# Performance work log

Measured on AMD Instinct MI355X. Metric: run time of the kernel, lower is better.

## Reference

```python
import jax, jax.numpy as jnp
import numpy as np

B, N, H, W, NHOR = 4096, 128, 128, 64, 3

def setup_inputs() -> dict:
    key = jax.random.key(0)
    ks = jax.random.split(key, 11)
    s = 1.0 / np.sqrt(H)
    return {
        "embeddings": jax.random.normal(ks[0], (B, H), jnp.float32),
        "sensor_embeddings": jax.random.normal(ks[1], (B, N, H), jnp.float32),
        "sensor_logits": jax.random.normal(ks[2], (B, N), jnp.float32),
        "fc1_w": jax.random.normal(ks[3], (H, H), jnp.float32) * s,
        "fc1_b": jax.random.normal(ks[4], (H,), jnp.float32) * s,
        "fc2_w": jax.random.normal(ks[5], (NHOR * N, H), jnp.float32) * s,
        "fc2_b": jax.random.normal(ks[6], (NHOR * N,), jnp.float32) * s,
        "rw1": jax.random.normal(ks[7], (N, H, H), jnp.float32) * s,
        "rb1": jax.random.normal(ks[8], (N, H), jnp.float32) * s,
        "rw2": jax.random.normal(ks[9], (N, H, W), jnp.float32) * s,
        "rb2": jax.random.normal(ks[10], (N, W), jnp.float32) * s,
    }

def reference(embeddings, sensor_embeddings, sensor_logits,
              fc1_w, fc1_b, fc2_w, fc2_b, rw1, rb1, rw2, rb2):
    # Forecasting head: Linear -> ReLU -> (Dropout: identity in eval) -> Linear
    h = jax.nn.relu(embeddings @ fc1_w.T + fc1_b)              # (B, H)
    forecast = (h @ fc2_w.T + fc2_b).reshape(-1, NHOR, N)      # (B, NHOR, N)
    # Reconstruction heads: per-node MLPs batched as stacked GEMMs
    hn = jax.nn.relu(jnp.einsum('bnh,nhk->bnk', sensor_embeddings, rw1) + rb1)  # (B, N, H)
    recon = jnp.einsum('bnk,nkw->bnw', hn, rw2) + rb2          # (B, N, W)
    reconstruction = jnp.transpose(recon, (0, 2, 1))           # (B, W, N), matches torch.stack(dim=2)
    return (sensor_logits, forecast, reconstruction)
```

## Files before the change

### kernel.cpp

```cpp
#include <hip/hip_runtime.h>
#include <hip/hip_bf16.h>
#include <stdint.h>

typedef __attribute__((ext_vector_type(8))) short bf16x8;
typedef __attribute__((ext_vector_type(4))) float f32x4;

#define DEVI static __device__ __forceinline__

static constexpr int B_SZ = 4096, N_SZ = 128, H_SZ = 128, W_SZ = 64;

static constexpr size_t OFF_W1 = 0;
static constexpr size_t OFF_W2 = OFF_W1 + 4194304;
static constexpr size_t OFF_F1 = OFF_W2 + 2097152;
static constexpr size_t OFF_F2 = OFF_F1 + 32768;
static constexpr size_t OFF_H  = OFF_F2 + 98304;

DEVI unsigned short f2bf(float f) {
  union { __hip_bfloat16 b; unsigned short u; } cv;
  cv.b = __float2bfloat16(f);
  return cv.u;
}
DEVI float bf2f(unsigned short u) {
  union { unsigned int i; float f; } cv;
  cv.i = ((unsigned int)u) << 16;
  return cv.f;
}

DEVI bf16x8 frag_ld(const unsigned char* base, int row, int kslot) {
  return *reinterpret_cast<const bf16x8*>(base + row * 256 + (((kslot ^ (row & 7)) << 4)));
}
DEVI bf16x8 gfrag_ld(const unsigned char* base, int row, int kslot) {
  return *reinterpret_cast<const bf16x8*>(base + row * 256 + (kslot << 4));
}

DEVI void stage_f32_tile(const float* src, int row_stride, unsigned char* dst, int tid, int nrows) {
  for (int t = tid; t < nrows * 16; t += 256) {
    int row = t >> 4, s = t & 15;
    const float* p = src + (size_t)row * row_stride + s * 8;
    union { unsigned short u[8]; uint4 v; } pk;
#pragma unroll
    for (int j = 0; j < 8; ++j) pk.u[j] = f2bf(p[j]);
    *reinterpret_cast<uint4*>(dst + row * 256 + ((s ^ (row & 7)) << 4)) = pk.v;
  }
}

__global__ __launch_bounds__(256) void prep_kernel(const float* __restrict__ rw1,
                                                   const float* __restrict__ rw2,
                                                   const float* __restrict__ fc1w,
                                                   const float* __restrict__ fc2w,
                                                   unsigned char* __restrict__ ws) {
  const int T_W1 = 128 * 128 * 16;
  const int T_W2 = 128 * 64 * 16;
  const int T_F1 = 128 * 16;
  const int T_F2 = 384 * 16;
  int id = blockIdx.x * 256 + threadIdx.x;
  if (id < T_W1) {
    int c = id & 127, rest = id >> 7;
    int s = rest & 15, n = rest >> 4;
    const float* src = rw1 + (size_t)n * 16384 + (size_t)(s * 8) * 128 + c;
    union { unsigned short u[8]; uint4 v; } pk;
#pragma unroll
    for (int j = 0; j < 8; ++j) pk.u[j] = f2bf(src[(size_t)j * 128]);
    size_t dst = OFF_W1 + ((size_t)n * 128 + c) * 256 + (size_t)(s << 4);
    *reinterpret_cast<uint4*>(ws + dst) = pk.v;
    return;
  }
  id -= T_W1;
  if (id < T_W2) {
    int w = id & 63, rest = id >> 6;
    int s = rest & 15, n = rest >> 4;
    const float* src = rw2 + (size_t)n * 8192 + (size_t)(s * 8) * 64 + w;
    union { unsigned short u[8]; uint4 v; } pk;
#pragma unroll
    for (int j = 0; j < 8; ++j) pk.u[j] = f2bf(src[(size_t)j * 64]);
    size_t dst = OFF_W2 + ((size_t)n * 64 + w) * 256 + (size_t)(s << 4);
    *reinterpret_cast<uint4*>(ws + dst) = pk.v;
    return;
  }
  id -= T_W2;
  if (id < T_F1) {
    int s = id & 15, o = id >> 4;
    const float* src = fc1w + (size_t)o * 128 + s * 8;
    union { unsigned short u[8]; uint4 v; } pk;
#pragma unroll
    for (int j = 0; j < 8; ++j) pk.u[j] = f2bf(src[j]);
    *reinterpret_cast<uint4*>(ws + OFF_F1 + (size_t)o * 256 + ((s ^ (o & 7)) << 4)) = pk.v;
    return;
  }
  id -= T_F1;
  if (id < T_F2) {
    int s = id & 15, o = id >> 4;
    const float* src = fc2w + (size_t)o * 128 + s * 8;
    union { unsigned short u[8]; uint4 v; } pk;
#pragma unroll
    for (int j = 0; j < 8; ++j) pk.u[j] = f2bf(src[j]);
    *reinterpret_cast<uint4*>(ws + OFF_F2 + (size_t)o * 256 + ((s ^ (o & 7)) << 4)) = pk.v;
  }
}

__global__ __launch_bounds__(256, 2) void recon_kernel(const float* __restrict__ se,
                                                       const float* __restrict__ rb1,
                                                       const float* __restrict__ rb2,
                                                       const unsigned char* __restrict__ ws,
                                                       float* __restrict__ out3) {
  __shared__ unsigned char sSE[2][16384];
  __shared__ unsigned char sHN[16384];

  const int tid = threadIdx.x;
  const int n = blockIdx.x;
  const int btg = blockIdx.y;
  const int b0 = btg * 512;

  const int wave = tid >> 6, lane = tid & 63;
  const int wm = wave >> 1, wq = wave & 1;
  const int lr = lane & 15, lk = lane >> 4;

  const unsigned char* w1b = ws + OFF_W1 + (size_t)n * 32768;
  const unsigned char* w2b = ws + OFF_W2 + (size_t)n * 16384;
  bf16x8 w1f[4][4], w2f[2][4];
#pragma unroll
  for (int m = 0; m < 4; ++m)
#pragma unroll
    for (int kk = 0; kk < 4; ++kk)
      w1f[m][kk] = gfrag_ld(w1b, wm * 64 + m * 16 + lr, kk * 4 + lk);
#pragma unroll
  for (int m = 0; m < 2; ++m)
#pragma unroll
    for (int kk = 0; kk < 4; ++kk)
      w2f[m][kk] = gfrag_ld(w2b, wm * 32 + m * 16 + lr, kk * 4 + lk);

  float bias1[4][4], bias2[2][4];
#pragma unroll
  for (int m = 0; m < 4; ++m)
#pragma unroll
    for (int j = 0; j < 4; ++j) bias1[m][j] = rb1[(size_t)n * 128 + wm * 64 + m * 16 + lk * 4 + j];
#pragma unroll
  for (int m = 0; m < 2; ++m)
#pragma unroll
    for (int j = 0; j < 4; ++j) bias2[m][j] = rb2[(size_t)n * 64 + wm * 32 + m * 16 + lk * 4 + j];

  stage_f32_tile(se + ((size_t)b0 * 128 + n) * 128, 128 * 128, sSE[0], tid, 64);
  unsigned short* outus = reinterpret_cast<unsigned short*>(out3);
  __syncthreads();

  float4 fra[4], frb[4];

  for (int t = 0; t < 8; ++t) {
    unsigned char* bufc = sSE[t & 1];
    unsigned char* bufn = sSE[(t + 1) & 1];

    if (t < 7) {
      const float* sb = se + ((size_t)(b0 + (t + 1) * 64) * 128 + n) * 128;
#pragma unroll
      for (int k = 0; k < 4; ++k) {
        int c = tid + k * 256;
        int row = c >> 4, s = c & 15;
        const float* p = sb + (size_t)row * 16384 + s * 8;
        fra[k] = *reinterpret_cast<const float4*>(p);
        frb[k] = *reinterpret_cast<const float4*>(p + 4);
      }
    }

    f32x4 acc[4][2] = {};
#pragma unroll
    for (int kk = 0; kk < 4; ++kk) {
      const int slot = kk * 4 + lk;
      bf16x8 bv[2];
#pragma unroll
      for (int q = 0; q < 2; ++q) bv[q] = frag_ld(bufc, wq * 32 + q * 16 + lr, slot);
#pragma unroll
      for (int m = 0; m < 4; ++m)
#pragma unroll
        for (int q = 0; q < 2; ++q)
          acc[m][q] = __builtin_amdgcn_mfma_f32_16x16x32_bf16(w1f[m][kk], bv[q], acc[m][q], 0, 0, 0);
    }

#pragma unroll
    for (int m = 0; m < 4; ++m) {
      const int k0 = wm * 64 + m * 16 + lk * 4;
      const int s16 = k0 >> 3, half = (k0 >> 2) & 1;
#pragma unroll
      for (int q = 0; q < 2; ++q) {
        const int b = wq * 32 + q * 16 + lr;
        union { unsigned short u[4]; uint2 v; } pk;
#pragma unroll
        for (int j = 0; j < 4; ++j) {
          float v = acc[m][q][j] + bias1[m][j];
          v = v > 0.f ? v : 0.f;
          pk.u[j] = f2bf(v);
        }
        *reinterpret_cast<uint2*>(sHN + b * 256 + ((s16 ^ (b & 7)) << 4) + half * 8) = pk.v;
      }
    }
    __syncthreads();

    f32x4 acc2[2][2] = {};
#pragma unroll
    for (int kk = 0; kk < 4; ++kk) {
      const int slot = kk * 4 + lk;
      bf16x8 bv[2];
#pragma unroll
      for (int q = 0; q < 2; ++q) bv[q] = frag_ld(sHN, wq * 32 + q * 16 + lr, slot);
#pragma unroll
      for (int m = 0; m < 2; ++m)
#pragma unroll
        for (int q = 0; q < 2; ++q)
          acc2[m][q] = __builtin_amdgcn_mfma_f32_16x16x32_bf16(w2f[m][kk], bv[q], acc2[m][q], 0, 0, 0);
    }

    if (t < 7) {
#pragma unroll
      for (int k = 0; k < 4; ++k) {
        int c = tid + k * 256;
        int row = c >> 4, s = c & 15;
        union { unsigned short u[8]; uint4 v; } pk;
#pragma unroll
        for (int j = 0; j < 4; ++j) pk.u[j] = f2bf(fra[k][j]);
#pragma unroll
        for (int j = 0; j < 4; ++j) pk.u[4 + j] = f2bf(frb[k][j]);
        *reinterpret_cast<uint4*>(bufn + row * 256 + ((s ^ (row & 7)) << 4)) = pk.v;
      }
    }

    const int bt0 = b0 + t * 64;
#pragma unroll
    for (int m = 0; m < 2; ++m) {
      const int w0 = wm * 32 + m * 16 + lk * 4;
#pragma unroll
      for (int q = 0; q < 2; ++q) {
        const int b = bt0 + wq * 32 + q * 16 + lr;
        union { unsigned short u[4]; uint2 v; } pk;
#pragma unroll
        for (int j = 0; j < 4; ++j) pk.u[j] = f2bf(acc2[m][q][j] + bias2[m][j]);
        *reinterpret_cast<uint2*>(outus + (size_t)b * 16384 + 8192 + n * 64 + w0) = pk.v;
      }
    }
    __syncthreads();
  }
}

__global__ __launch_bounds__(256) void transpose_kernel(float* __restrict__ out3) {
  const int b = blockIdx.x, wave = threadIdx.x >> 6, lane = threadIdx.x & 63;
  const unsigned short* t = reinterpret_cast<const unsigned short*>(out3) + (size_t)b * 16384 + 8192;
  float* dst = out3 + (size_t)b * 8192;
  uint4 r[2][2];
#pragma unroll
  for (int half = 0; half < 2; ++half) {
    const int g = half * 4 + wave;
    r[half][0] = *reinterpret_cast<const uint4*>(t + lane * 64 + g * 8);
    r[half][1] = *reinterpret_cast<const uint4*>(t + (size_t)(lane + 64) * 64 + g * 8);
  }
  __syncthreads();
#pragma unroll
  for (int half = 0; half < 2; ++half) {
    const int g = half * 4 + wave;
    union { uint4 v; unsigned short u[8]; } p0, p1;
    p0.v = r[half][0];
    p1.v = r[half][1];
#pragma unroll
    for (int j = 0; j < 8; ++j) {
      dst[(g * 8 + j) * 128 + lane] = bf2f(p0.u[j]);
      dst[(g * 8 + j) * 128 + lane + 64] = bf2f(p1.u[j]);
    }
  }
}

__global__ __launch_bounds__(256) void f1_kernel(const float* __restrict__ emb,
                                                 const float* __restrict__ fc1b,
                                                 const unsigned char* __restrict__ ws,
                                                 unsigned char* __restrict__ hsw) {
  __shared__ unsigned char sA[32768];
  __shared__ unsigned char sB[32768];
  const int tid = threadIdx.x;
  const int bt = blockIdx.x;
  const int b0 = bt * 128;
  {
    const uint4* wp = reinterpret_cast<const uint4*>(ws + OFF_F1);
    uint4* d = reinterpret_cast<uint4*>(sB);
    for (int c = tid; c < 2048; c += 256) d[c] = wp[c];
  }
  stage_f32_tile(emb + (size_t)b0 * 128, 128, sA, tid, 128);
  __syncthreads();

  const int wave = tid >> 6, lane = tid & 63;
  const int wm = wave >> 1, wn = wave & 1;
  const int lr = lane & 15, lk = lane >> 4;

  f32x4 acc[4][4] = {};
#pragma unroll
  for (int kk = 0; kk < 4; ++kk) {
    bf16x8 af[4], bfv[4];
#pragma unroll
    for (int m = 0; m < 4; ++m) af[m] = frag_ld(sA, wm * 64 + m * 16 + lr, kk * 4 + lk);
#pragma unroll
    for (int q = 0; q < 4; ++q) bfv[q] = frag_ld(sB, wn * 64 + q * 16 + lr, kk * 4 + lk);
#pragma unroll
    for (int m = 0; m < 4; ++m)
#pragma unroll
      for (int q = 0; q < 4; ++q)
        acc[m][q] = __builtin_amdgcn_mfma_f32_16x16x32_bf16(af[m], bfv[q], acc[m][q], 0, 0, 0);
  }

  unsigned char* tile = hsw + (size_t)bt * 32768;
#pragma unroll
  for (int q = 0; q < 4; ++q) {
    int c = wn * 64 + q * 16 + lr;
    float bias = fc1b[c];
#pragma unroll
    for (int m = 0; m < 4; ++m) {
#pragma unroll
      for (int j = 0; j < 4; ++j) {
        int r = wm * 64 + m * 16 + lk * 4 + j;
        float v = acc[m][q][j] + bias;
        v = v > 0.f ? v : 0.f;
        *reinterpret_cast<unsigned short*>(tile + r * 256 + ((c * 2) ^ ((r & 7) << 4))) = f2bf(v);
      }
    }
  }
}

__global__ __launch_bounds__(256) void f2_kernel(const unsigned char* __restrict__ hsw,
                                                 const unsigned char* __restrict__ f2s,
                                                 const float* __restrict__ fc2b,
                                                 float* __restrict__ out2) {
  __shared__ unsigned char sA[32768];
  __shared__ unsigned char sB[32768];
  const int tid = threadIdx.x;
  const int bt = blockIdx.x;
  const int ch = blockIdx.y;
  const int b0 = bt * 128;
  {
    const uint4* ap = reinterpret_cast<const uint4*>(hsw + (size_t)bt * 32768);
    uint4* da = reinterpret_cast<uint4*>(sA);
    for (int c = tid; c < 2048; c += 256) da[c] = ap[c];
    const uint4* bp = reinterpret_cast<const uint4*>(f2s + (size_t)ch * 32768);
    uint4* db = reinterpret_cast<uint4*>(sB);
    for (int c = tid; c < 2048; c += 256) db[c] = bp[c];
  }
  __syncthreads();

  const int wave = tid >> 6, lane = tid & 63;
  const int wm = wave >> 1, wn = wave & 1;
  const int lr = lane & 15, lk = lane >> 4;

  f32x4 acc[4][4] = {};
#pragma unroll
  for (int kk = 0; kk < 4; ++kk) {
    bf16x8 af[4], bfv[4];
#pragma unroll
    for (int m = 0; m < 4; ++m) af[m] = frag_ld(sA, wm * 64 + m * 16 + lr, kk * 4 + lk);
#pragma unroll
    for (int q = 0; q < 4; ++q) bfv[q] = frag_ld(sB, wn * 64 + q * 16 + lr, kk * 4 + lk);
#pragma unroll
    for (int m = 0; m < 4; ++m)
#pragma unroll
      for (int q = 0; q < 4; ++q)
        acc[m][q] = __builtin_amdgcn_mfma_f32_16x16x32_bf16(af[m], bfv[q], acc[m][q], 0, 0, 0);
  }

#pragma unroll
  for (int q = 0; q < 4; ++q) {
    int o = ch * 128 + wn * 64 + q * 16 + lr;
    float bias = fc2b[o];
#pragma unroll
    for (int m = 0; m < 4; ++m) {
#pragma unroll
      for (int j = 0; j < 4; ++j) {
        int r = wm * 64 + m * 16 + lk * 4 + j;
        out2[(size_t)(b0 + r) * 384 + o] = acc[m][q][j] + bias;
      }
    }
  }
}

extern "C" void kernel_launch(void* const* d_in, const int* in_sizes, int n_in,
                              void* d_out, int out_size, void* d_ws, size_t ws_size,
                              hipStream_t stream) {
  const float* emb  = (const float*)d_in[0];
  const float* se   = (const float*)d_in[1];
  const float* slog = (const float*)d_in[2];
  const float* fc1w = (const float*)d_in[3];
  const float* fc1b = (const float*)d_in[4];
  const float* fc2w = (const float*)d_in[5];
  const float* fc2b = (const float*)d_in[6];
  const float* rw1  = (const float*)d_in[7];
  const float* rb1  = (const float*)d_in[8];
  const float* rw2  = (const float*)d_in[9];
  const float* rb2  = (const float*)d_in[10];
  float* out = (float*)d_out;
  unsigned char* ws = (unsigned char*)d_ws;

  hipMemcpyAsync(out, slog, (size_t)B_SZ * N_SZ * sizeof(float),
                 hipMemcpyDeviceToDevice, stream);

  prep_kernel<<<1568, 256, 0, stream>>>(rw1, rw2, fc1w, fc2w, ws);

  f1_kernel<<<32, 256, 0, stream>>>(emb, fc1b, ws, ws + OFF_H);
  f2_kernel<<<dim3(32, 3), 256, 0, stream>>>(ws + OFF_H, ws + OFF_F2, fc2b,
                                             out + (size_t)B_SZ * N_SZ);

  float* out3 = out + (size_t)B_SZ * N_SZ + (size_t)B_SZ * 384;
  recon_kernel<<<dim3(128, 8), 256, 0, stream>>>(se, rb1, rb2, ws, out3);
  transpose_kernel<<<4096, 256, 0, stream>>>(out3);
}
```

Measured before the change: 140.9 us.

## Fuse reconstruction transpose into recon kernel via per-block node-chunk tiling

The recon kernel now handles 4 consecutive nodes for a 64-row batch tile, not one node across 512 batch rows. Results are staged in a new 32KB shared buffer laid out as (batch, w, node). It then writes the transposed fp32 output directly as float4 stores, which removes the separate transpose kernel and its bf16 intermediate round-trip through global memory. In exchange, weights are reloaded per node with less reuse across batch rows, the SE buffer is single-buffered with extra barriers, and shared memory use grows, which may lower occupancy.

```diff
diff --git a/kernel.cpp b/kernel.cpp
--- a/kernel.cpp
+++ b/kernel.cpp
@@ -103,63 +103,79 @@
                                                        const float* __restrict__ rb2,
                                                        const unsigned char* __restrict__ ws,
                                                        float* __restrict__ out3) {
-  __shared__ unsigned char sSE[2][16384];
+  __shared__ unsigned char sSE[16384];
   __shared__ unsigned char sHN[16384];
+  __shared__ unsigned char sOUT[32768];
 
   const int tid = threadIdx.x;
-  const int n = blockIdx.x;
-  const int btg = blockIdx.y;
-  const int b0 = btg * 512;
+  const int id = blockIdx.x;
+  const int chunk = ((id & 7) << 2) | ((id >> 3) & 3);
+  const int btile = id >> 5;
+  const int n0 = chunk * 4;
+  const int b0 = btile * 64;
 
   const int wave = tid >> 6, lane = tid & 63;
   const int wm = wave >> 1, wq = wave & 1;
   const int lr = lane & 15, lk = lane >> 4;
 
-  const unsigned char* w1b = ws + OFF_W1 + (size_t)n * 32768;
-  const unsigned char* w2b = ws + OFF_W2 + (size_t)n * 16384;
-  bf16x8 w1f[4][4], w2f[2][4];
-#pragma unroll
-  for (int m = 0; m < 4; ++m)
-#pragma unroll
-    for (int kk = 0; kk < 4; ++kk)
-      w1f[m][kk] = gfrag_ld(w1b, wm * 64 + m * 16 + lr, kk * 4 + lk);
-#pragma unroll
-  for (int m = 0; m < 2; ++m)
-#pragma unroll
-    for (int kk = 0; kk < 4; ++kk)
-      w2f[m][kk] = gfrag_ld(w2b, wm * 32 + m * 16 + lr, kk * 4 + lk);
-
-  float bias1[4][4], bias2[2][4];
-#pragma unroll
-  for (int m = 0; m < 4; ++m)
-#pragma unroll
-    for (int j = 0; j < 4; ++j) bias1[m][j] = rb1[(size_t)n * 128 + wm * 64 + m * 16 + lk * 4 + j];
-#pragma unroll
-  for (int m = 0; m < 2; ++m)
-#pragma unroll
-    for (int j = 0; j < 4; ++j) bias2[m][j] = rb2[(size_t)n * 64 + wm * 32 + m * 16 + lk * 4 + j];
-
-  stage_f32_tile(se + ((size_t)b0 * 128 + n) * 128, 128 * 128, sSE[0], tid, 64);
-  unsigned short* outus = reinterpret_cast<unsigned short*>(out3);
+  stage_f32_tile(se + ((size_t)b0 * 128 + n0) * 128, 128 * 128, sSE, tid, 64);
   __syncthreads();
 
   float4 fra[4], frb[4];
 
-  for (int t = 0; t < 8; ++t) {
-    unsigned char* bufc = sSE[t & 1];
-    unsigned char* bufn = sSE[(t + 1) & 1];
-
-    if (t < 7) {
-      const float* sb = se + ((size_t)(b0 + (t + 1) * 64) * 128 + n) * 128;
-#pragma unroll
-      for (int k = 0; k < 4; ++k) {
-        int c = tid + k * 256;
-        int row = c >> 4, s = c & 15;
-        const float* p = sb + (size_t)row * 16384 + s * 8;
-        fra[k] = *reinterpret_cast<const float4*>(p);
-        frb[k] = *reinterpret_cast<const float4*>(p + 4);
-      }
-    }
+  auto issue_pref = [&](int n) {
+    const float* sb = se + ((size_t)b0 * 128 + n) * 128;
+#pragma unroll
+    for (int k = 0; k < 4; ++k) {
+      int c = tid + k * 256;
+      int row = c >> 4, s = c & 15;
+      const float* p = sb + (size_t)row * 16384 + s * 8;
+      fra[k] = *reinterpret_cast<const float4*>(p);
+      frb[k] = *reinterpret_cast<const float4*>(p + 4);
+    }
+  };
+  auto write_pref = [&]() {
+#pragma unroll
+    for (int k = 0; k < 4; ++k) {
+      int c = tid + k * 256;
+      int row = c >> 4, s = c & 15;
+      union { unsigned short u[8]; uint4 v; } pk;
+#pragma unroll
+      for (int j = 0; j < 4; ++j) pk.u[j] = f2bf(fra[k][j]);
+#pragma unroll
+      for (int j = 0; j < 4; ++j) pk.u[4 + j] = f2bf(frb[k][j]);
+      *reinterpret_cast<uint4*>(sSE + row * 256 + ((s ^ (row & 7)) << 4)) = pk.v;
+    }
+  };
+
+#pragma unroll 1
+  for (int nl = 0; nl < 4; ++nl) {
+    const int n = n0 + nl;
+
+    const unsigned char* w1b = ws + OFF_W1 + (size_t)n * 32768;
+    const unsigned char* w2b = ws + OFF_W2 + (size_t)n * 16384;
+    bf16x8 w1f[4][4], w2f[2][4];
+#pragma unroll
+    for (int m = 0; m < 4; ++m)
+#pragma unroll
+      for (int kk = 0; kk < 4; ++kk)
+        w1f[m][kk] = gfrag_ld(w1b, wm * 64 + m * 16 + lr, kk * 4 + lk);
+#pragma unroll
+    for (int m = 0; m < 2; ++m)
+#pragma unroll
+      for (int kk = 0; kk < 4; ++kk)
+        w2f[m][kk] = gfrag_ld(w2b, wm * 32 + m * 16 + lr, kk * 4 + lk);
+    float bias1[4][4], bias2[2][4];
+#pragma unroll
+    for (int m = 0; m < 4; ++m)
+#pragma unroll
+      for (int j = 0; j < 4; ++j) bias1[m][j] = rb1[(size_t)n * 128 + wm * 64 + m * 16 + lk * 4 + j];
+#pragma unroll
+    for (int m = 0; m < 2; ++m)
+#pragma unroll
+      for (int j = 0; j < 4; ++j) bias2[m][j] = rb2[(size_t)n * 64 + wm * 32 + m * 16 + lk * 4 + j];
+
+    if (nl == 0) issue_pref(n0 + 1);
 
     f32x4 acc[4][2] = {};
 #pragma unroll
@@ -167,13 +183,14 @@
       const int slot = kk * 4 + lk;
       bf16x8 bv[2];
 #pragma unroll
-      for (int q = 0; q < 2; ++q) bv[q] = frag_ld(bufc, wq * 32 + q * 16 + lr, slot);
+      for (int q = 0; q < 2; ++q) bv[q] = frag_ld(sSE, wq * 32 + q * 16 + lr, slot);
 #pragma unroll
       for (int m = 0; m < 4; ++m)
 #pragma unroll
         for (int q = 0; q < 2; ++q)
           acc[m][q] = __builtin_amdgcn_mfma_f32_16x16x32_bf16(w1f[m][kk], bv[q], acc[m][q], 0, 0, 0);
     }
+    __syncthreads();
 
 #pragma unroll
     for (int m = 0; m < 4; ++m) {
@@ -192,7 +209,11 @@
         *reinterpret_cast<uint2*>(sHN + b * 256 + ((s16 ^ (b & 7)) << 4) + half * 8) = pk.v;
       }
     }
+
+    if (nl < 3) write_pref();
     __syncthreads();
+
+    if (nl < 2) issue_pref(n0 + nl + 2);
 
     f32x4 acc2[2][2] = {};
 #pragma unroll
@@ -208,59 +229,36 @@
           acc2[m][q] = __builtin_amdgcn_mfma_f32_16x16x32_bf16(w2f[m][kk], bv[q], acc2[m][q], 0, 0, 0);
     }
 
-    if (t < 7) {
-#pragma unroll
-      for (int k = 0; k < 4; ++k) {
-        int c = tid + k * 256;
-        int row = c >> 4, s = c & 15;
-        union { unsigned short u[8]; uint4 v; } pk;
-#pragma unroll
-        for (int j = 0; j < 4; ++j) pk.u[j] = f2bf(fra[k][j]);
-#pragma unroll
-        for (int j = 0; j < 4; ++j) pk.u[4 + j] = f2bf(frb[k][j]);
-        *reinterpret_cast<uint4*>(bufn + row * 256 + ((s ^ (row & 7)) << 4)) = pk.v;
+#pragma unroll
+    for (int m = 0; m < 2; ++m) {
+#pragma unroll
+      for (int q = 0; q < 2; ++q) {
+        const int b = wq * 32 + q * 16 + lr;
+#pragma unroll
+        for (int j = 0; j < 4; ++j) {
+          const int w = wm * 32 + m * 16 + lk * 4 + j;
+          float v = acc2[m][q][j] + bias2[m][j];
+          *reinterpret_cast<unsigned short*>(sOUT + b * 512 + ((w ^ (b & 7)) << 3) + nl * 2) = f2bf(v);
+        }
       }
     }
-
-    const int bt0 = b0 + t * 64;
-#pragma unroll
-    for (int m = 0; m < 2; ++m) {
-      const int w0 = wm * 32 + m * 16 + lk * 4;
-#pragma unroll
-      for (int q = 0; q < 2; ++q) {
-        const int b = bt0 + wq * 32 + q * 16 + lr;
-        union { unsigned short u[4]; uint2 v; } pk;
-#pragma unroll
-        for (int j = 0; j < 4; ++j) pk.u[j] = f2bf(acc2[m][q][j] + bias2[m][j]);
-        *reinterpret_cast<uint2*>(outus + (size_t)b * 16384 + 8192 + n * 64 + w0) = pk.v;
-      }
-    }
-    __syncthreads();
-  }
-}
-
-__global__ __launch_bounds__(256) void transpose_kernel(float* __restrict__ out3) {
-  const int b = blockIdx.x, wave = threadIdx.x >> 6, lane = threadIdx.x & 63;
-  const unsigned short* t = reinterpret_cast<const unsigned short*>(out3) + (size_t)b * 16384 + 8192;
-  float* dst = out3 + (size_t)b * 8192;
-  uint4 r[2][2];
-#pragma unroll
-  for (int half = 0; half < 2; ++half) {
-    const int g = half * 4 + wave;
-    r[half][0] = *reinterpret_cast<const uint4*>(t + lane * 64 + g * 8);
-    r[half][1] = *reinterpret_cast<const uint4*>(t + (size_t)(lane + 64) * 64 + g * 8);
   }
   __syncthreads();
-#pragma unroll
-  for (int half = 0; half < 2; ++half) {
-    const int g = half * 4 + wave;
-    union { uint4 v; unsigned short u[8]; } p0, p1;
-    p0.v = r[half][0];
-    p1.v = r[half][1];
-#pragma unroll
-    for (int j = 0; j < 8; ++j) {
-      dst[(g * 8 + j) * 128 + lane] = bf2f(p0.u[j]);
-      dst[(g * 8 + j) * 128 + lane + 64] = bf2f(p1.u[j]);
+
+  {
+    const int w = lane;
+    float* dst = out3 + (size_t)b0 * 8192 + w * 128 + n0;
+#pragma unroll
+    for (int bb = 0; bb < 16; ++bb) {
+      const int b = wave * 16 + bb;
+      union { uint2 v; unsigned short u[4]; } rd;
+      rd.v = *reinterpret_cast<const uint2*>(sOUT + b * 512 + ((w ^ (b & 7)) << 3));
+      float4 o;
+      o.x = bf2f(rd.u[0]);
+      o.y = bf2f(rd.u[1]);
+      o.z = bf2f(rd.u[2]);
+      o.w = bf2f(rd.u[3]);
+      *reinterpret_cast<float4*>(dst + (size_t)b * 8192) = o;
     }
   }
 }
@@ -400,6 +398,5 @@
                                              out + (size_t)B_SZ * N_SZ);
 
   float* out3 = out + (size_t)B_SZ * N_SZ + (size_t)B_SZ * 384;
-  recon_kernel<<<dim3(128, 8), 256, 0, stream>>>(se, rb1, rb2, ws, out3);
-  transpose_kernel<<<4096, 256, 0, stream>>>(out3);
-}
+  recon_kernel<<<2048, 256, 0, stream>>>(se, rb1, rb2, ws, out3);
+}
```

New measurement: 216.1 us. 53.4% more time.
